# Optimization experiments

Measured on AMD Instinct MI355X. Metric: run time of the kernel, lower is better.

Reference implementation:

```python
import jax, jax.numpy as jnp
import numpy as np

B, N, HIST, PRED = 32, 4096, 16, 8
IN_DIM, HID, GCN_OUT, E = 10, 32, 2, 65536


def setup_inputs() -> dict:
    key = jax.random.key(0)
    ks = jax.random.split(key, 11)
    s = 0.15  # keep gate pre-activations in a sane range
    return {
        "pm25_hist": jax.random.normal(ks[0], (B, HIST, N), jnp.float32),
        "feature": jax.random.normal(ks[1], (B, HIST + PRED, N, IN_DIM - 1), jnp.float32),
        "edge_index": jax.random.randint(ks[2], (2, E), 0, N, dtype=jnp.int32),
        "cheb_w": jax.random.normal(ks[3], (2, IN_DIM, GCN_OUT), jnp.float32) * s,
        "cheb_b": jax.random.normal(ks[4], (GCN_OUT,), jnp.float32) * s,
        "x2h_w": jax.random.normal(ks[5], (IN_DIM + GCN_OUT, 4 * HID), jnp.float32) * s,
        "x2h_b": jax.random.normal(ks[6], (4 * HID,), jnp.float32) * s,
        "h2h_w": jax.random.normal(ks[7], (HID, 4 * HID), jnp.float32) * s,
        "h2h_b": jax.random.normal(ks[8], (4 * HID,), jnp.float32) * s,
        "fc_w": jax.random.normal(ks[9], (HID, 1), jnp.float32) * s,
        "fc_b": jax.random.normal(ks[10], (1,), jnp.float32) * s,
    }


def _cheb_norm(edge_index):
    # PyG ChebConv(K=2, sym norm, lambda_max=2): Tx1 = -D^{-1/2} A D^{-1/2} x, zero diagonal
    src, dst = edge_index[0], edge_index[1]
    deg = jnp.zeros((N,), jnp.float32).at[src].add(1.0)
    dis = jnp.where(deg > 0, jax.lax.rsqrt(jnp.maximum(deg, 1e-12)), 0.0)
    return -dis[src] * dis[dst], src, dst


def _cheb_conv(x, src, dst, norm, W, b):
    # x: [B,N,F]; message x[src] aggregated at dst
    msg = x[:, src, :] * norm[None, :, None]
    tx1 = jnp.zeros_like(x[..., :1].repeat(x.shape[-1], -1)).at[:, dst, :].add(msg)
    return jnp.einsum("bnf,fo->bno", x, W[0]) + jnp.einsum("bnf,fo->bno", tx1, W[1]) + b


def _lstm(x, h, c, x2h_w, x2h_b, h2h_w, h2h_b):
    g = x @ x2h_w + x2h_b + h @ h2h_w + h2h_b  # [B,N,4H]
    i, f, gc, o = jnp.split(g, 4, axis=-1)
    c = jax.nn.sigmoid(f) * c + jax.nn.sigmoid(i) * jnp.tanh(gc)
    h = jax.nn.sigmoid(o) * jnp.tanh(c)
    return h, c


def reference(pm25_hist, feature, edge_index, cheb_w, cheb_b, x2h_w, x2h_b, h2h_w, h2h_b, fc_w, fc_b):
    norm, src, dst = _cheb_norm(edge_index)

    def step(carry, x):
        h, c = carry
        xg = jax.nn.sigmoid(_cheb_conv(x, src, dst, norm, cheb_w, cheb_b))
        h, c = _lstm(jnp.concatenate([x, xg], -1), h, c, x2h_w, x2h_b, h2h_w, h2h_b)
        return (h, c), None

    h = jnp.zeros((B, N, HID), jnp.float32)
    c = jnp.zeros((B, N, HID), jnp.float32)

    # history phase
    xs_hist = jnp.concatenate([pm25_hist[..., None], feature[:, :HIST]], -1)  # [B,HIST,N,10]
    (h, c), _ = jax.lax.scan(step, (h, c), jnp.swapaxes(xs_hist, 0, 1))
    xn = h @ fc_w + fc_b  # [B,N,1]

    # prediction phase (recurrent through xn)
    def pred_step(carry, feat_t):
        h, c, xn = carry
        x = jnp.concatenate([xn, feat_t], -1)  # [B,N,10]
        (h, c), _ = step((h, c), x)
        xn = h @ fc_w + fc_b
        return (h, c, xn), xn

    _, ys = jax.lax.scan(pred_step, (h, c, xn), jnp.swapaxes(feature[:, HIST:], 0, 1))
    return jnp.squeeze(jnp.swapaxes(ys, 0, 1), -1)  # [B,PRED,N]
```

## Files before the change

kernel.cpp:

```cpp
#include <hip/hip_runtime.h>
#include <math.h>

#define Bb    32
#define Nn    4096
#define HISTC 16
#define PREDC 8
#define TTC   24
#define EC    65536
#define BN    (Bb*Nn)

typedef float f32x2 __attribute__((ext_vector_type(2)));
typedef float f32x4 __attribute__((ext_vector_type(4)));
typedef __fp16 f16x8 __attribute__((ext_vector_type(8)));
typedef __fp16 fp16v2 __attribute__((ext_vector_type(2)));

__device__ __forceinline__ float sigm_f(float x){
  return __builtin_amdgcn_rcpf(1.f + __expf(-x));
}
__device__ __forceinline__ float tanh_f(float x){
  return fmaf(-2.f, __builtin_amdgcn_rcpf(1.f + __expf(2.f*x)), 1.f);
}
__device__ __forceinline__ unsigned pk2(float a, float b){
  fp16v2 v = __builtin_amdgcn_cvt_pkrtz(a, b);
  return __builtin_bit_cast(unsigned, v);
}
__device__ __forceinline__ f32x4 mfma16(uint4 a, uint4 b, f32x4 c){
  return __builtin_amdgcn_mfma_f32_16x16x32_f16(
      __builtin_bit_cast(f16x8, a), __builtin_bit_cast(f16x8, b), c, 0, 0, 0);
}

__global__ void k_deg(const int* __restrict__ ei, int* deg, int* cnt){
  int e = blockIdx.x*blockDim.x + threadIdx.x;
  if (e < EC){ atomicAdd(&deg[ei[e]],1); atomicAdd(&cnt[ei[EC+e]],1); }
}
__global__ void k_dis(const int* __restrict__ deg, float* dis){
  int n = blockIdx.x*blockDim.x + threadIdx.x;
  if (n < Nn) dis[n] = deg[n] > 0 ? rsqrtf((float)deg[n]) : 0.f;
}
__global__ void k_scan(const int* __restrict__ cnt, int* ptr){
  __shared__ int sd[1024];
  int t = threadIdx.x;
  int c0=cnt[4*t], c1=cnt[4*t+1], c2=cnt[4*t+2], c3=cnt[4*t+3];
  int s = c0+c1+c2+c3;
  sd[t] = s; __syncthreads();
  for (int off=1; off<1024; off<<=1){
    int v = (t>=off) ? sd[t-off] : 0;
    __syncthreads();
    sd[t] += v;
    __syncthreads();
  }
  int excl = sd[t]-s;
  ptr[4*t]=excl; ptr[4*t+1]=excl+c0; ptr[4*t+2]=excl+c0+c1; ptr[4*t+3]=excl+c0+c1+c2;
  if (t==1023) ptr[4096]=sd[1023];
}
__global__ void k_fill(const int* __restrict__ ei, const float* __restrict__ dis,
                       const int* __restrict__ ptr, int* fillc, int2* __restrict__ epack){
  int e = blockIdx.x*blockDim.x + threadIdx.x;
  if (e < EC){
    int s = ei[e], d = ei[EC+e];
    int pos = ptr[d] + atomicAdd(&fillc[d],1);
    epack[pos] = make_int2(s, __float_as_int(-dis[s]*dis[d]));
  }
}

__global__ void k_prep(const float* __restrict__ x2hw, const float* __restrict__ h2hw,
                       const float* __restrict__ x2hb, const float* __restrict__ h2hb,
                       _Float16* __restrict__ wfrag){
  int i = blockIdx.x*256 + threadIdx.x;
  int f = i >> 9, lane = (i >> 3) & 63, j = i & 7;
  int kt = f >> 3, ct = f & 7;
  int k = kt*32 + (lane>>4)*8 + j;
  int col = ct*16 + (lane&15);
  float v;
  if (k < 12)       v = x2hw[k*128 + col];
  else if (k == 12) v = x2hb[col] + h2hb[col];
  else if (k < 32)  v = 0.f;
  else              v = h2hw[(k-32)*128 + col];
  wfrag[f*512 + lane*8 + j] = (_Float16)v;
}

__global__ __launch_bounds__(256)
void k_zh(const float* __restrict__ pm25, const float* __restrict__ feat,
          const float* __restrict__ cw, f32x2* __restrict__ zbufH){
  int r = blockIdx.x*256 + threadIdx.x;
  int t = r >> 17, bn = r & (BN-1);
  int b = bn >> 12, n = bn & (Nn-1);
  const float* fp = feat + ((size_t)(b*TTC + t)*Nn + n)*9;
  float x[10];
  x[0] = pm25[(size_t)(b*HISTC + t)*Nn + n];
  #pragma unroll
  for (int f=0;f<9;++f) x[1+f] = fp[f];
  float z0=0.f, z1=0.f;
  #pragma unroll
  for (int f=0;f<10;++f){
    z0 += x[f]*cw[20+f*2+0]; z1 += x[f]*cw[20+f*2+1];
  }
  zbufH[((size_t)(t*Bb + b))*Nn + n] = (f32x2){z0, z1};
}

__global__ __launch_bounds__(256)
void k_tr(const f32x2* __restrict__ in, f32x2* __restrict__ out, int R, int C){
  __shared__ f32x2 tile[64][65];
  int tilesR = R >> 6;
  int br = blockIdx.x % tilesR, bc = blockIdx.x / tilesR;
  int r0 = br << 6, c0 = bc << 6;
  for (int i=threadIdx.x; i<4096; i+=256){
    int r = i>>6, c = i&63;
    tile[r][c] = in[(size_t)(r0+r)*C + c0+c];
  }
  __syncthreads();
  for (int i=threadIdx.x; i<4096; i+=256){
    int r = i>>6, c = i&63;
    out[(size_t)(c0+r)*R + r0+c] = tile[c][r];
  }
}

__global__ __launch_bounds__(256)
void k_agg(const int* __restrict__ ptr, const int2* __restrict__ epack,
           const float4* __restrict__ zT, float4* __restrict__ aggT){
  int n = blockIdx.x;
  int tid = threadIdx.x;
  int p0 = ptr[n], p1 = ptr[n+1];
  f32x4 acc = {0.f,0.f,0.f,0.f};
  int i = p0;
  for (; i+1 < p1; i += 2){
    int2 e0 = epack[i], e1 = epack[i+1];
    float w0 = __int_as_float(e0.y), w1 = __int_as_float(e1.y);
    float4 z0 = zT[(size_t)e0.x*256 + tid];
    float4 z1 = zT[(size_t)e1.x*256 + tid];
    acc.x = fmaf(w0, z0.x, acc.x); acc.y = fmaf(w0, z0.y, acc.y);
    acc.z = fmaf(w0, z0.z, acc.z); acc.w = fmaf(w0, z0.w, acc.w);
    acc.x = fmaf(w1, z1.x, acc.x); acc.y = fmaf(w1, z1.y, acc.y);
    acc.z = fmaf(w1, z1.z, acc.z); acc.w = fmaf(w1, z1.w, acc.w);
  }
  if (i < p1){
    int2 e = epack[i];
    float w = __int_as_float(e.y);
    float4 z = zT[(size_t)e.x*256 + tid];
    acc.x = fmaf(w, z.x, acc.x); acc.y = fmaf(w, z.y, acc.y);
    acc.z = fmaf(w, z.z, acc.z); acc.w = fmaf(w, z.w, acc.w);
  }
  aggT[(size_t)n*256 + tid] = make_float4(acc.x, acc.y, acc.z, acc.w);
}

__global__ __launch_bounds__(256)
void k_zf(const float* __restrict__ feat, const float* __restrict__ cw,
          f32x2* __restrict__ zf){
  int r = blockIdx.x*256 + threadIdx.x;
  int tp = r >> 17, bn = r & (BN-1);
  int b = bn >> 12, n = bn & (Nn-1);
  int t = HISTC + tp;
  const float* fp = feat + ((size_t)(b*TTC + t)*Nn + n)*9;
  float z0=0.f, z1=0.f;
  #pragma unroll
  for (int f=0;f<9;++f){
    float v = fp[f];
    z0 += v*cw[20+(f+1)*2+0]; z1 += v*cw[20+(f+1)*2+1];
  }
  zf[((size_t)(tp*Bb + b))*Nn + n] = (f32x2){z0, z1};
}

#define POINTWISE(r)                                                            \
  c0[r] = fmaf(sigm_f(acc[0][r]), tanh_f(acc[4][r]), sigm_f(acc[2][r])*c0[r]);  \
  h0[r] = sigm_f(acc[6][r])*tanh_f(c0[r]);                                      \
  c1[r] = fmaf(sigm_f(acc[1][r]), tanh_f(acc[5][r]), sigm_f(acc[3][r])*c1[r]);  \
  h1[r] = sigm_f(acc[7][r])*tanh_f(c1[r]);

__global__ __launch_bounds__(256,1)
void k_hist(const float* __restrict__ pm25, const float* __restrict__ feat,
            const f32x2* __restrict__ aggH,
            const float* __restrict__ cw, const float* __restrict__ cb,
            const uint4* __restrict__ wfrag,
            const float* __restrict__ fcw, const float* __restrict__ fcb,
            uint4* __restrict__ hfragO, float4* __restrict__ cO,
            float* __restrict__ xn0){
  __shared__ __align__(16) _Float16 hl[4][16][40];
  int tid = threadIdx.x;
  int lane = tid & 63, w = tid >> 6;
  int gw = blockIdx.x*4 + w;
  int r0 = gw*16;
  int b = r0 >> 12, n0 = r0 & (Nn-1);
  int l15 = lane & 15, g4 = lane >> 4;
  int nrow = n0 + l15;
  const float* pb = pm25 + (size_t)b*HISTC*Nn + nrow;
  const float* fb = feat + ((size_t)b*TTC*Nn + nrow)*9;

  uint4 bw[16];
  #pragma unroll
  for (int f=0; f<16; ++f) bw[f] = wfrag[f*64 + lane];
  float fw0 = fcw[l15], fw1 = fcw[l15+16];

  uint4 ah = make_uint4(0,0,0,0);
  float c0[4]={0,0,0,0}, c1[4]={0,0,0,0};
  float h0[4], h1[4];
  const f32x4 zacc = {0.f,0.f,0.f,0.f};

  #pragma unroll 1
  for (int t=0; t<HISTC; ++t){
    const float* fbt = fb + (size_t)t*Nn*9;
    float xv[9]; float a0 = 0.f, a1 = 0.f; float x0 = 0.f;
    if (g4 == 0){
      x0 = pb[(size_t)t*Nn];
      #pragma unroll
      for (int f=0;f<7;++f) xv[f] = fbt[f];
      a0 = x0*cw[0]; a1 = x0*cw[1];
      #pragma unroll
      for (int f=0;f<7;++f){ a0 += xv[f]*cw[(f+1)*2]; a1 += xv[f]*cw[(f+1)*2+1]; }
    } else if (g4 == 1){
      xv[7] = fbt[7]; xv[8] = fbt[8];
      a0 = cb[0] + xv[7]*cw[16] + xv[8]*cw[18];
      a1 = cb[1] + xv[7]*cw[17] + xv[8]*cw[19];
    } else if (g4 == 2){
      f32x2 ag = aggH[((size_t)(t*Bb + b))*Nn + nrow];
      a0 = ag.x; a1 = ag.y;
    }
    a0 += __shfl_xor(a0, 16); a0 += __shfl_xor(a0, 32);
    a1 += __shfl_xor(a1, 16); a1 += __shfl_xor(a1, 32);
    float xg0 = sigm_f(a0), xg1 = sigm_f(a1);

    uint4 ax;
    if (g4 == 0){
      ax.x = pk2(x0, xv[0]);     ax.y = pk2(xv[1], xv[2]);
      ax.z = pk2(xv[3], xv[4]);  ax.w = pk2(xv[5], xv[6]);
    } else if (g4 == 1){
      ax.x = pk2(xv[7], xv[8]);  ax.y = pk2(xg0, xg1);
      ax.z = pk2(1.f, 0.f);      ax.w = 0u;
    } else {
      ax = make_uint4(0,0,0,0);
    }

    f32x4 acc[8];
    #pragma unroll
    for (int ct=0; ct<8; ++ct) acc[ct] = mfma16(ax, bw[ct], zacc);
    #pragma unroll
    for (int ct=0; ct<8; ++ct) acc[ct] = mfma16(ah, bw[8+ct], acc[ct]);

    POINTWISE(0) POINTWISE(1) POINTWISE(2) POINTWISE(3)

    #pragma unroll
    for (int r=0;r<4;++r){
      hl[w][g4*4+r][l15]    = (_Float16)h0[r];
      hl[w][g4*4+r][l15+16] = (_Float16)h1[r];
    }
    asm volatile("s_waitcnt lgkmcnt(0)" ::: "memory");
    ah = *(const uint4*)&hl[w][l15][g4*8];
  }

  hfragO[(size_t)gw*64 + lane] = ah;
  cO[((size_t)gw*64 + lane)*2]   = make_float4(c0[0],c0[1],c0[2],c0[3]);
  cO[((size_t)gw*64 + lane)*2+1] = make_float4(c1[0],c1[1],c1[2],c1[3]);
  #pragma unroll
  for (int r=0;r<4;++r){
    float p = fmaf(h0[r], fw0, h1[r]*fw1);
    p += __shfl_xor(p, 1, 16); p += __shfl_xor(p, 2, 16);
    p += __shfl_xor(p, 4, 16); p += __shfl_xor(p, 8, 16);
    if (l15 == 0) xn0[r0 + g4*4 + r] = p + fcb[0];
  }
}

__global__ __launch_bounds__(256,1)
void k_pred_cell(const float* __restrict__ feat, const float* __restrict__ xnI,
                 const f32x2* __restrict__ zft,
                 const int* __restrict__ ptr, const int2* __restrict__ epack,
                 const float* __restrict__ cw, const float* __restrict__ cb,
                 const uint4* __restrict__ wfrag,
                 const float* __restrict__ fcw, const float* __restrict__ fcb,
                 uint4* __restrict__ hfrag, float4* __restrict__ cS,
                 float* __restrict__ xnO, float* __restrict__ out, int t){
  __shared__ f32x2 zl2[Nn];
  __shared__ __align__(16) _Float16 hl[4][16][40];
  int tid = threadIdx.x;
  int lane = tid & 63, w = tid >> 6;
  int gw = blockIdx.x*4 + w;
  int r0 = gw*16;
  int b = r0 >> 12, n0 = r0 & (Nn-1);
  int l15 = lane & 15, g4 = lane >> 4;

  {
    const f32x2* zsrc = zft + (size_t)b*Nn;
    const float* xb = xnI + (size_t)b*Nn;
    float w10 = cw[20], w11 = cw[21];
    #pragma unroll
    for (int k=0;k<16;++k){
      int idx = tid + k*256;
      f32x2 z = zsrc[idx];
      float xnv = xb[idx];
      zl2[idx] = (f32x2){fmaf(xnv, w10, z.x), fmaf(xnv, w11, z.y)};
    }
  }

  uint4 bw[16];
  #pragma unroll
  for (int f=0; f<16; ++f) bw[f] = wfrag[f*64 + lane];
  float fw0 = fcw[l15], fw1 = fcw[l15+16];

  uint4 ah = hfrag[(size_t)gw*64 + lane];
  float4 cv0 = cS[((size_t)gw*64 + lane)*2];
  float4 cv1 = cS[((size_t)gw*64 + lane)*2+1];
  float c0[4] = {cv0.x, cv0.y, cv0.z, cv0.w};
  float c1[4] = {cv1.x, cv1.y, cv1.z, cv1.w};
  float h0[4], h1[4];
  const f32x4 zacc = {0.f,0.f,0.f,0.f};

  int nrow = n0 + l15;
  const float* fbt = feat + ((size_t)(b*TTC + t)*Nn + n0 + l15)*9;
  float xv[9]; float a0 = 0.f, a1 = 0.f; float x0 = 0.f;
  if (g4 == 0){
    x0 = xnI[r0 + l15];
    #pragma unroll
    for (int f=0;f<7;++f) xv[f] = fbt[f];
    a0 = x0*cw[0]; a1 = x0*cw[1];
    #pragma unroll
    for (int f=0;f<7;++f){ a0 += xv[f]*cw[(f+1)*2]; a1 += xv[f]*cw[(f+1)*2+1]; }
  } else if (g4 == 1){
    xv[7] = fbt[7]; xv[8] = fbt[8];
    a0 = cb[0] + xv[7]*cw[16] + xv[8]*cw[18];
    a1 = cb[1] + xv[7]*cw[17] + xv[8]*cw[19];
  }

  __syncthreads();

  {
    int p0 = ptr[nrow], p1 = ptr[nrow+1];
    for (int i = p0 + g4; i < p1; i += 4){
      int2 e = epack[i];
      float wgt = __int_as_float(e.y);
      f32x2 zv = zl2[e.x];
      a0 = fmaf(wgt, zv.x, a0);
      a1 = fmaf(wgt, zv.y, a1);
    }
    a0 += __shfl_xor(a0, 16); a0 += __shfl_xor(a0, 32);
    a1 += __shfl_xor(a1, 16); a1 += __shfl_xor(a1, 32);
  }
  float xg0 = sigm_f(a0), xg1 = sigm_f(a1);

  uint4 ax;
  if (g4 == 0){
    ax.x = pk2(x0, xv[0]);     ax.y = pk2(xv[1], xv[2]);
    ax.z = pk2(xv[3], xv[4]);  ax.w = pk2(xv[5], xv[6]);
  } else if (g4 == 1){
    ax.x = pk2(xv[7], xv[8]);  ax.y = pk2(xg0, xg1);
    ax.z = pk2(1.f, 0.f);      ax.w = 0u;
  } else {
    ax = make_uint4(0,0,0,0);
  }

  f32x4 acc[8];
  #pragma unroll
  for (int ct=0; ct<8; ++ct) acc[ct] = mfma16(ax, bw[ct], zacc);
  #pragma unroll
  for (int ct=0; ct<8; ++ct) acc[ct] = mfma16(ah, bw[8+ct], acc[ct]);

  POINTWISE(0) POINTWISE(1) POINTWISE(2) POINTWISE(3)

  #pragma unroll
  for (int r=0;r<4;++r){
    hl[w][g4*4+r][l15]    = (_Float16)h0[r];
    hl[w][g4*4+r][l15+16] = (_Float16)h1[r];
  }
  asm volatile("s_waitcnt lgkmcnt(0)" ::: "memory");
  ah = *(const uint4*)&hl[w][l15][g4*8];

  hfrag[(size_t)gw*64 + lane] = ah;
  cS[((size_t)gw*64 + lane)*2]   = make_float4(c0[0],c0[1],c0[2],c0[3]);
  cS[((size_t)gw*64 + lane)*2+1] = make_float4(c1[0],c1[1],c1[2],c1[3]);
  #pragma unroll
  for (int r=0;r<4;++r){
    float p = fmaf(h0[r], fw0, h1[r]*fw1);
    p += __shfl_xor(p, 1, 16); p += __shfl_xor(p, 2, 16);
    p += __shfl_xor(p, 4, 16); p += __shfl_xor(p, 8, 16);
    if (l15 == 0){
      float rr = p + fcb[0];
      int nr = n0 + g4*4 + r;
      xnO[r0 + g4*4 + r] = rr;
      out[(size_t)b*PREDC*Nn + nr] = rr;
    }
  }
}

extern "C" void kernel_launch(void* const* d_in, const int* in_sizes, int n_in,
                              void* d_out, int out_size, void* d_ws, size_t ws_size,
                              hipStream_t stream){
  const float* pm25 = (const float*)d_in[0];
  const float* feat = (const float*)d_in[1];
  const int*   ei   = (const int*)d_in[2];
  const float* cw   = (const float*)d_in[3];
  const float* cb   = (const float*)d_in[4];
  const float* x2hw = (const float*)d_in[5];
  const float* x2hb = (const float*)d_in[6];
  const float* h2hw = (const float*)d_in[7];
  const float* h2hb = (const float*)d_in[8];
  const float* fcw  = (const float*)d_in[9];
  const float* fcb  = (const float*)d_in[10];
  float* out = (float*)d_out;

  char* w = (char*)d_ws;
  size_t off = 0;
  auto take = [&](size_t bytes)->char*{
    char* r = w + off; off += (bytes + 255) & ~(size_t)255; return r;
  };
  int*      deg   = (int*)      take(Nn*4);
  int*      cnt   = (int*)      take(Nn*4);
  int*      fillc = (int*)      take(Nn*4);
  int*      ptr   = (int*)      take((Nn+1)*4);
  float*    dis   = (float*)    take(Nn*4);
  int2*     epack = (int2*)     take(EC*8);
  _Float16* wfrag = (_Float16*) take(16*512*2);
  f32x2*    bufA  = (f32x2*)    take((size_t)HISTC*BN*8);
  f32x2*    bufB  = (f32x2*)    take((size_t)HISTC*BN*8);
  f32x2*    zf    = (f32x2*)    take((size_t)PREDC*BN*8);
  uint4*    hfrag = (uint4*)    take((size_t)(BN/16)*64*16);
  float4*   cbuf  = (float4*)   take((size_t)(BN/16)*64*2*16);
  float*    xn0   = (float*)    take((size_t)BN*4);
  float*    xn1   = (float*)    take((size_t)BN*4);

  (void)hipMemsetAsync(deg, 0, Nn*4*3, stream);

  k_deg <<<EC/256, 256, 0, stream>>>(ei, deg, cnt);
  k_dis <<<Nn/256, 256, 0, stream>>>(deg, dis);
  k_scan<<<1, 1024, 0, stream>>>(cnt, ptr);
  k_fill<<<EC/256, 256, 0, stream>>>(ei, dis, ptr, fillc, epack);
  k_prep<<<32, 256, 0, stream>>>(x2hw, h2hw, x2hb, h2hb, wfrag);

  k_zh<<<(HISTC*BN)/256, 256, 0, stream>>>(pm25, feat, cw, bufA);
  k_tr<<<512, 256, 0, stream>>>(bufA, bufB, 512, Nn);
  k_agg<<<Nn, 256, 0, stream>>>(ptr, epack, (const float4*)bufB, (float4*)bufA);
  k_tr<<<512, 256, 0, stream>>>(bufA, bufB, Nn, 512);

  k_hist<<<BN/64, 256, 0, stream>>>(pm25, feat, bufB, cw, cb,
                                    (const uint4*)wfrag, fcw, fcb,
                                    hfrag, cbuf, xn0);

  k_zf<<<(PREDC*BN)/256, 256, 0, stream>>>(feat, cw, zf);
  for (int tp = 0; tp < PREDC; ++tp){
    int t = HISTC + tp;
    float* xi = (tp & 1) ? xn1 : xn0;
    float* xo = (tp & 1) ? xn0 : xn1;
    k_pred_cell<<<BN/64, 256, 0, stream>>>(feat, xi, zf + (size_t)tp*BN,
                                           ptr, epack, cw, cb,
                                           (const uint4*)wfrag, fcw, fcb,
                                           hfrag, cbuf, xo, out + (size_t)tp*Nn, t);
  }
}
```

Before: 436.2 us.

## Precompute feature-part graph aggregation for prediction steps and aggregate only xn per step

Uses linearity of the Chebyshev aggregation to split each prediction step's graph term into a feature part and an xn part. The feature part is computed for all 8 prediction steps in one batched transpose/aggregate pass alongside the history steps, and each step then only aggregates the scalar xn via a small k_aggx kernel using a transposed xn layout. This replaces the per-block shared-memory z staging and edge loop in k_pred_cell. k_hist now processes two row tiles per wave, and buffers are aliased to cut workspace size, at the cost of an extra kernel launch per prediction step.

```diff
diff --git a/kernel.cpp b/kernel.cpp
--- a/kernel.cpp
+++ b/kernel.cpp
@@ -8,6 +8,7 @@
 #define TTC   24
 #define EC    65536
 #define BN    (Bb*Nn)
+#define NSL   768
 
 typedef float f32x2 __attribute__((ext_vector_type(2)));
 typedef float f32x4 __attribute__((ext_vector_type(4)));
@@ -81,7 +82,7 @@
 
 __global__ __launch_bounds__(256)
 void k_zh(const float* __restrict__ pm25, const float* __restrict__ feat,
-          const float* __restrict__ cw, f32x2* __restrict__ zbufH){
+          const float* __restrict__ cw, f32x2* __restrict__ zAll){
   int r = blockIdx.x*256 + threadIdx.x;
   int t = r >> 17, bn = r & (BN-1);
   int b = bn >> 12, n = bn & (Nn-1);
@@ -95,7 +96,24 @@
   for (int f=0;f<10;++f){
     z0 += x[f]*cw[20+f*2+0]; z1 += x[f]*cw[20+f*2+1];
   }
-  zbufH[((size_t)(t*Bb + b))*Nn + n] = (f32x2){z0, z1};
+  zAll[((size_t)(t*Bb + b))*Nn + n] = (f32x2){z0, z1};
+}
+
+__global__ __launch_bounds__(256)
+void k_zf(const float* __restrict__ feat, const float* __restrict__ cw,
+          f32x2* __restrict__ zAll){
+  int r = blockIdx.x*256 + threadIdx.x;
+  int tp = r >> 17, bn = r & (BN-1);
+  int b = bn >> 12, n = bn & (Nn-1);
+  int t = HISTC + tp;
+  const float* fp = feat + ((size_t)(b*TTC + t)*Nn + n)*9;
+  float z0=0.f, z1=0.f;
+  #pragma unroll
+  for (int f=0;f<9;++f){
+    float v = fp[f];
+    z0 += v*cw[20+(f+1)*2+0]; z1 += v*cw[20+(f+1)*2+1];
+  }
+  zAll[((size_t)(512 + tp*Bb + b))*Nn + n] = (f32x2){z0, z1};
 }
 
 __global__ __launch_bounds__(256)
@@ -115,19 +133,20 @@
   }
 }
 
-__global__ __launch_bounds__(256)
-void k_agg(const int* __restrict__ ptr, const int2* __restrict__ epack,
-           const float4* __restrict__ zT, float4* __restrict__ aggT){
-  int n = blockIdx.x;
-  int tid = threadIdx.x;
+__global__ __launch_bounds__(64)
+void k_aggc(const int* __restrict__ ptr, const int2* __restrict__ epack,
+            const float4* __restrict__ zT, float4* __restrict__ aggT){
+  int n  = blockIdx.x & (Nn-1);
+  int cb = blockIdx.x >> 12;
+  int col = cb*64 + threadIdx.x;
   int p0 = ptr[n], p1 = ptr[n+1];
   f32x4 acc = {0.f,0.f,0.f,0.f};
   int i = p0;
   for (; i+1 < p1; i += 2){
     int2 e0 = epack[i], e1 = epack[i+1];
     float w0 = __int_as_float(e0.y), w1 = __int_as_float(e1.y);
-    float4 z0 = zT[(size_t)e0.x*256 + tid];
-    float4 z1 = zT[(size_t)e1.x*256 + tid];
+    float4 z0 = zT[(size_t)e0.x*384 + col];
+    float4 z1 = zT[(size_t)e1.x*384 + col];
     acc.x = fmaf(w0, z0.x, acc.x); acc.y = fmaf(w0, z0.y, acc.y);
     acc.z = fmaf(w0, z0.z, acc.z); acc.w = fmaf(w0, z0.w, acc.w);
     acc.x = fmaf(w1, z1.x, acc.x); acc.y = fmaf(w1, z1.y, acc.y);
@@ -136,28 +155,27 @@
   if (i < p1){
     int2 e = epack[i];
     float w = __int_as_float(e.y);
-    float4 z = zT[(size_t)e.x*256 + tid];
+    float4 z = zT[(size_t)e.x*384 + col];
     acc.x = fmaf(w, z.x, acc.x); acc.y = fmaf(w, z.y, acc.y);
     acc.z = fmaf(w, z.z, acc.z); acc.w = fmaf(w, z.w, acc.w);
   }
-  aggT[(size_t)n*256 + tid] = make_float4(acc.x, acc.y, acc.z, acc.w);
+  aggT[(size_t)n*384 + col] = make_float4(acc.x, acc.y, acc.z, acc.w);
 }
 
 __global__ __launch_bounds__(256)
-void k_zf(const float* __restrict__ feat, const float* __restrict__ cw,
-          f32x2* __restrict__ zf){
-  int r = blockIdx.x*256 + threadIdx.x;
-  int tp = r >> 17, bn = r & (BN-1);
-  int b = bn >> 12, n = bn & (Nn-1);
-  int t = HISTC + tp;
-  const float* fp = feat + ((size_t)(b*TTC + t)*Nn + n)*9;
-  float z0=0.f, z1=0.f;
-  #pragma unroll
-  for (int f=0;f<9;++f){
-    float v = fp[f];
-    z0 += v*cw[20+(f+1)*2+0]; z1 += v*cw[20+(f+1)*2+1];
-  }
-  zf[((size_t)(tp*Bb + b))*Nn + n] = (f32x2){z0, z1};
+void k_aggx(const int* __restrict__ ptr, const int2* __restrict__ epack,
+            const float* __restrict__ xnT, float* __restrict__ aggx){
+  int lane = threadIdx.x & 63, w = threadIdx.x >> 6;
+  int n = blockIdx.x*4 + w;
+  int b = lane & 31, half = lane >> 5;
+  int p0 = ptr[n], p1 = ptr[n+1];
+  float acc = 0.f;
+  for (int i = p0 + half; i < p1; i += 2){
+    int2 e = epack[i];
+    acc = fmaf(__int_as_float(e.y), xnT[(size_t)e.x*32 + b], acc);
+  }
+  acc += __shfl_xor(acc, 32);
+  if (lane < 32) aggx[(size_t)b*Nn + n] = acc;
 }
 
 #define POINTWISE(r)                                                            \
@@ -173,7 +191,110 @@
             const uint4* __restrict__ wfrag,
             const float* __restrict__ fcw, const float* __restrict__ fcb,
             uint4* __restrict__ hfragO, float4* __restrict__ cO,
-            float* __restrict__ xn0){
+            float* __restrict__ xn0, float* __restrict__ xnT){
+  __shared__ __align__(16) _Float16 hl[4][16][40];
+  int tid = threadIdx.x;
+  int lane = tid & 63, w = tid >> 6;
+  int gw0 = blockIdx.x*4 + w;
+  int l15 = lane & 15, g4 = lane >> 4;
+
+  uint4 bw[16];
+  #pragma unroll
+  for (int f=0; f<16; ++f) bw[f] = wfrag[f*64 + lane];
+  float fw0 = fcw[l15], fw1 = fcw[l15+16];
+  const f32x4 zacc = {0.f,0.f,0.f,0.f};
+
+  #pragma unroll 1
+  for (int tt=0; tt<2; ++tt){
+    int gw = gw0 + tt*4096;
+    int r0 = gw*16;
+    int b = r0 >> 12, n0 = r0 & (Nn-1);
+    int nrow = n0 + l15;
+    const float* pb = pm25 + (size_t)b*HISTC*Nn + nrow;
+    const float* fb = feat + ((size_t)b*TTC*Nn + nrow)*9;
+
+    uint4 ah = make_uint4(0,0,0,0);
+    float c0[4]={0,0,0,0}, c1[4]={0,0,0,0};
+    float h0[4], h1[4];
+
+    #pragma unroll 1
+    for (int t=0; t<HISTC; ++t){
+      const float* fbt = fb + (size_t)t*Nn*9;
+      float xv[9]; float a0 = 0.f, a1 = 0.f; float x0 = 0.f;
+      if (g4 == 0){
+        x0 = pb[(size_t)t*Nn];
+        #pragma unroll
+        for (int f=0;f<7;++f) xv[f] = fbt[f];
+        a0 = x0*cw[0]; a1 = x0*cw[1];
+        #pragma unroll
+        for (int f=0;f<7;++f){ a0 += xv[f]*cw[(f+1)*2]; a1 += xv[f]*cw[(f+1)*2+1]; }
+      } else if (g4 == 1){
+        xv[7] = fbt[7]; xv[8] = fbt[8];
+        a0 = cb[0] + xv[7]*cw[16] + xv[8]*cw[18];
+        a1 = cb[1] + xv[7]*cw[17] + xv[8]*cw[19];
+      } else if (g4 == 2){
+        f32x2 ag = aggH[((size_t)(t*Bb + b))*Nn + nrow];
+        a0 = ag.x; a1 = ag.y;
+      }
+      a0 += __shfl_xor(a0, 16); a0 += __shfl_xor(a0, 32);
+      a1 += __shfl_xor(a1, 16); a1 += __shfl_xor(a1, 32);
+      float xg0 = sigm_f(a0), xg1 = sigm_f(a1);
+
+      uint4 ax;
+      if (g4 == 0){
+        ax.x = pk2(x0, xv[0]);     ax.y = pk2(xv[1], xv[2]);
+        ax.z = pk2(xv[3], xv[4]);  ax.w = pk2(xv[5], xv[6]);
+      } else if (g4 == 1){
+        ax.x = pk2(xv[7], xv[8]);  ax.y = pk2(xg0, xg1);
+        ax.z = pk2(1.f, 0.f);      ax.w = 0u;
+      } else {
+        ax = make_uint4(0,0,0,0);
+      }
+
+      f32x4 acc[8];
+      #pragma unroll
+      for (int ct=0; ct<8; ++ct) acc[ct] = mfma16(ax, bw[ct], zacc);
+      #pragma unroll
+      for (int ct=0; ct<8; ++ct) acc[ct] = mfma16(ah, bw[8+ct], acc[ct]);
+
+      POINTWISE(0) POINTWISE(1) POINTWISE(2) POINTWISE(3)
+
+      #pragma unroll
+      for (int r=0;r<4;++r){
+        hl[w][g4*4+r][l15]    = (_Float16)h0[r];
+        hl[w][g4*4+r][l15+16] = (_Float16)h1[r];
+      }
+      asm volatile("s_waitcnt lgkmcnt(0)" ::: "memory");
+      ah = *(const uint4*)&hl[w][l15][g4*8];
+    }
+
+    hfragO[(size_t)gw*64 + lane] = ah;
+    cO[((size_t)gw*64 + lane)*2]   = make_float4(c0[0],c0[1],c0[2],c0[3]);
+    cO[((size_t)gw*64 + lane)*2+1] = make_float4(c1[0],c1[1],c1[2],c1[3]);
+    #pragma unroll
+    for (int r=0;r<4;++r){
+      float p = fmaf(h0[r], fw0, h1[r]*fw1);
+      p += __shfl_xor(p, 1, 16); p += __shfl_xor(p, 2, 16);
+      p += __shfl_xor(p, 4, 16); p += __shfl_xor(p, 8, 16);
+      if (l15 == 0){
+        float rr = p + fcb[0];
+        int nr = n0 + g4*4 + r;
+        xn0[r0 + g4*4 + r] = rr;
+        xnT[(size_t)nr*32 + b] = rr;
+      }
+    }
+  }
+}
+
+__global__ __launch_bounds__(256,1)
+void k_pred_cell(const float* __restrict__ feat, float* __restrict__ xn0,
+                 const f32x2* __restrict__ aggzf,
+                 const float* __restrict__ aggx,
+                 const float* __restrict__ cw, const float* __restrict__ cb,
+                 const uint4* __restrict__ wfrag,
+                 const float* __restrict__ fcw, const float* __restrict__ fcb,
+                 uint4* __restrict__ hfrag, float4* __restrict__ cS,
+                 float* __restrict__ xnT, float* __restrict__ out, int t){
   __shared__ __align__(16) _Float16 hl[4][16][40];
   int tid = threadIdx.x;
   int lane = tid & 63, w = tid >> 6;
@@ -182,112 +303,6 @@
   int b = r0 >> 12, n0 = r0 & (Nn-1);
   int l15 = lane & 15, g4 = lane >> 4;
   int nrow = n0 + l15;
-  const float* pb = pm25 + (size_t)b*HISTC*Nn + nrow;
-  const float* fb = feat + ((size_t)b*TTC*Nn + nrow)*9;
-
-  uint4 bw[16];
-  #pragma unroll
-  for (int f=0; f<16; ++f) bw[f] = wfrag[f*64 + lane];
-  float fw0 = fcw[l15], fw1 = fcw[l15+16];
-
-  uint4 ah = make_uint4(0,0,0,0);
-  float c0[4]={0,0,0,0}, c1[4]={0,0,0,0};
-  float h0[4], h1[4];
-  const f32x4 zacc = {0.f,0.f,0.f,0.f};
-
-  #pragma unroll 1
-  for (int t=0; t<HISTC; ++t){
-    const float* fbt = fb + (size_t)t*Nn*9;
-    float xv[9]; float a0 = 0.f, a1 = 0.f; float x0 = 0.f;
-    if (g4 == 0){
-      x0 = pb[(size_t)t*Nn];
-      #pragma unroll
-      for (int f=0;f<7;++f) xv[f] = fbt[f];
-      a0 = x0*cw[0]; a1 = x0*cw[1];
-      #pragma unroll
-      for (int f=0;f<7;++f){ a0 += xv[f]*cw[(f+1)*2]; a1 += xv[f]*cw[(f+1)*2+1]; }
-    } else if (g4 == 1){
-      xv[7] = fbt[7]; xv[8] = fbt[8];
-      a0 = cb[0] + xv[7]*cw[16] + xv[8]*cw[18];
-      a1 = cb[1] + xv[7]*cw[17] + xv[8]*cw[19];
-    } else if (g4 == 2){
-      f32x2 ag = aggH[((size_t)(t*Bb + b))*Nn + nrow];
-      a0 = ag.x; a1 = ag.y;
-    }
-    a0 += __shfl_xor(a0, 16); a0 += __shfl_xor(a0, 32);
-    a1 += __shfl_xor(a1, 16); a1 += __shfl_xor(a1, 32);
-    float xg0 = sigm_f(a0), xg1 = sigm_f(a1);
-
-    uint4 ax;
-    if (g4 == 0){
-      ax.x = pk2(x0, xv[0]);     ax.y = pk2(xv[1], xv[2]);
-      ax.z = pk2(xv[3], xv[4]);  ax.w = pk2(xv[5], xv[6]);
-    } else if (g4 == 1){
-      ax.x = pk2(xv[7], xv[8]);  ax.y = pk2(xg0, xg1);
-      ax.z = pk2(1.f, 0.f);      ax.w = 0u;
-    } else {
-      ax = make_uint4(0,0,0,0);
-    }
-
-    f32x4 acc[8];
-    #pragma unroll
-    for (int ct=0; ct<8; ++ct) acc[ct] = mfma16(ax, bw[ct], zacc);
-    #pragma unroll
-    for (int ct=0; ct<8; ++ct) acc[ct] = mfma16(ah, bw[8+ct], acc[ct]);
-
-    POINTWISE(0) POINTWISE(1) POINTWISE(2) POINTWISE(3)
-
-    #pragma unroll
-    for (int r=0;r<4;++r){
-      hl[w][g4*4+r][l15]    = (_Float16)h0[r];
-      hl[w][g4*4+r][l15+16] = (_Float16)h1[r];
-    }
-    asm volatile("s_waitcnt lgkmcnt(0)" ::: "memory");
-    ah = *(const uint4*)&hl[w][l15][g4*8];
-  }
-
-  hfragO[(size_t)gw*64 + lane] = ah;
-  cO[((size_t)gw*64 + lane)*2]   = make_float4(c0[0],c0[1],c0[2],c0[3]);
-  cO[((size_t)gw*64 + lane)*2+1] = make_float4(c1[0],c1[1],c1[2],c1[3]);
-  #pragma unroll
-  for (int r=0;r<4;++r){
-    float p = fmaf(h0[r], fw0, h1[r]*fw1);
-    p += __shfl_xor(p, 1, 16); p += __shfl_xor(p, 2, 16);
-    p += __shfl_xor(p, 4, 16); p += __shfl_xor(p, 8, 16);
-    if (l15 == 0) xn0[r0 + g4*4 + r] = p + fcb[0];
-  }
-}
-
-__global__ __launch_bounds__(256,1)
-void k_pred_cell(const float* __restrict__ feat, const float* __restrict__ xnI,
-                 const f32x2* __restrict__ zft,
-                 const int* __restrict__ ptr, const int2* __restrict__ epack,
-                 const float* __restrict__ cw, const float* __restrict__ cb,
-                 const uint4* __restrict__ wfrag,
-                 const float* __restrict__ fcw, const float* __restrict__ fcb,
-                 uint4* __restrict__ hfrag, float4* __restrict__ cS,
-                 float* __restrict__ xnO, float* __restrict__ out, int t){
-  __shared__ f32x2 zl2[Nn];
-  __shared__ __align__(16) _Float16 hl[4][16][40];
-  int tid = threadIdx.x;
-  int lane = tid & 63, w = tid >> 6;
-  int gw = blockIdx.x*4 + w;
-  int r0 = gw*16;
-  int b = r0 >> 12, n0 = r0 & (Nn-1);
-  int l15 = lane & 15, g4 = lane >> 4;
-
-  {
-    const f32x2* zsrc = zft + (size_t)b*Nn;
-    const float* xb = xnI + (size_t)b*Nn;
-    float w10 = cw[20], w11 = cw[21];
-    #pragma unroll
-    for (int k=0;k<16;++k){
-      int idx = tid + k*256;
-      f32x2 z = zsrc[idx];
-      float xnv = xb[idx];
-      zl2[idx] = (f32x2){fmaf(xnv, w10, z.x), fmaf(xnv, w11, z.y)};
-    }
-  }
 
   uint4 bw[16];
   #pragma unroll
@@ -302,11 +317,10 @@
   float h0[4], h1[4];
   const f32x4 zacc = {0.f,0.f,0.f,0.f};
 
-  int nrow = n0 + l15;
-  const float* fbt = feat + ((size_t)(b*TTC + t)*Nn + n0 + l15)*9;
+  const float* fbt = feat + ((size_t)(b*TTC + t)*Nn + nrow)*9;
   float xv[9]; float a0 = 0.f, a1 = 0.f; float x0 = 0.f;
   if (g4 == 0){
-    x0 = xnI[r0 + l15];
+    x0 = xn0[r0 + l15];
     #pragma unroll
     for (int f=0;f<7;++f) xv[f] = fbt[f];
     a0 = x0*cw[0]; a1 = x0*cw[1];
@@ -316,22 +330,14 @@
     xv[7] = fbt[7]; xv[8] = fbt[8];
     a0 = cb[0] + xv[7]*cw[16] + xv[8]*cw[18];
     a1 = cb[1] + xv[7]*cw[17] + xv[8]*cw[19];
-  }
-
-  __syncthreads();
-
-  {
-    int p0 = ptr[nrow], p1 = ptr[nrow+1];
-    for (int i = p0 + g4; i < p1; i += 4){
-      int2 e = epack[i];
-      float wgt = __int_as_float(e.y);
-      f32x2 zv = zl2[e.x];
-      a0 = fmaf(wgt, zv.x, a0);
-      a1 = fmaf(wgt, zv.y, a1);
-    }
-    a0 += __shfl_xor(a0, 16); a0 += __shfl_xor(a0, 32);
-    a1 += __shfl_xor(a1, 16); a1 += __shfl_xor(a1, 32);
-  }
+  } else if (g4 == 2){
+    f32x2 azf = aggzf[(size_t)b*Nn + nrow];
+    float axv = aggx[(size_t)b*Nn + nrow];
+    a0 = fmaf(cw[20], axv, azf.x);
+    a1 = fmaf(cw[21], axv, azf.y);
+  }
+  a0 += __shfl_xor(a0, 16); a0 += __shfl_xor(a0, 32);
+  a1 += __shfl_xor(a1, 16); a1 += __shfl_xor(a1, 32);
   float xg0 = sigm_f(a0), xg1 = sigm_f(a1);
 
   uint4 ax;
@@ -372,7 +378,8 @@
     if (l15 == 0){
       float rr = p + fcb[0];
       int nr = n0 + g4*4 + r;
-      xnO[r0 + g4*4 + r] = rr;
+      xn0[r0 + g4*4 + r] = rr;
+      xnT[(size_t)nr*32 + b] = rr;
       out[(size_t)b*PREDC*Nn + nr] = rr;
     }
   }
@@ -394,10 +401,10 @@
   const float* fcb  = (const float*)d_in[10];
   float* out = (float*)d_out;
 
-  char* w = (char*)d_ws;
+  char* wsp = (char*)d_ws;
   size_t off = 0;
   auto take = [&](size_t bytes)->char*{
-    char* r = w + off; off += (bytes + 255) & ~(size_t)255; return r;
+    char* r = wsp + off; off += (bytes + 255) & ~(size_t)255; return r;
   };
   int*      deg   = (int*)      take(Nn*4);
   int*      cnt   = (int*)      take(Nn*4);
@@ -406,13 +413,16 @@
   float*    dis   = (float*)    take(Nn*4);
   int2*     epack = (int2*)     take(EC*8);
   _Float16* wfrag = (_Float16*) take(16*512*2);
-  f32x2*    bufA  = (f32x2*)    take((size_t)HISTC*BN*8);
-  f32x2*    bufB  = (f32x2*)    take((size_t)HISTC*BN*8);
-  f32x2*    zf    = (f32x2*)    take((size_t)PREDC*BN*8);
-  uint4*    hfrag = (uint4*)    take((size_t)(BN/16)*64*16);
-  float4*   cbuf  = (float4*)   take((size_t)(BN/16)*64*2*16);
+  char*     bufA  =             take((size_t)NSL*Nn*8);
+  char*     bufB  =             take((size_t)NSL*Nn*8);
   float*    xn0   = (float*)    take((size_t)BN*4);
-  float*    xn1   = (float*)    take((size_t)BN*4);
+  float*    xnT   = (float*)    take((size_t)BN*4);
+  float*    aggx  = (float*)    take((size_t)BN*4);
+
+  f32x2* zAll = (f32x2*)bufA;
+  f32x2* zT   = (f32x2*)bufB;
+  uint4*  hfrag = (uint4*)bufA;
+  float4* cbuf  = (float4*)(bufA + (size_t)8388608);
 
   (void)hipMemsetAsync(deg, 0, Nn*4*3, stream);
 
@@ -422,23 +432,24 @@
   k_fill<<<EC/256, 256, 0, stream>>>(ei, dis, ptr, fillc, epack);
   k_prep<<<32, 256, 0, stream>>>(x2hw, h2hw, x2hb, h2hb, wfrag);
 
-  k_zh<<<(HISTC*BN)/256, 256, 0, stream>>>(pm25, feat, cw, bufA);
-  k_tr<<<512, 256, 0, stream>>>(bufA, bufB, 512, Nn);
-  k_agg<<<Nn, 256, 0, stream>>>(ptr, epack, (const float4*)bufB, (float4*)bufA);
-  k_tr<<<512, 256, 0, stream>>>(bufA, bufB, Nn, 512);
-
-  k_hist<<<BN/64, 256, 0, stream>>>(pm25, feat, bufB, cw, cb,
-                                    (const uint4*)wfrag, fcw, fcb,
-                                    hfrag, cbuf, xn0);
-
-  k_zf<<<(PREDC*BN)/256, 256, 0, stream>>>(feat, cw, zf);
+  k_zh<<<(HISTC*BN)/256, 256, 0, stream>>>(pm25, feat, cw, zAll);
+  k_zf<<<(PREDC*BN)/256, 256, 0, stream>>>(feat, cw, zAll);
+  k_tr<<<(NSL/64)*(Nn/64), 256, 0, stream>>>(zAll, zT, NSL, Nn);
+  k_aggc<<<6*Nn, 64, 0, stream>>>(ptr, epack, (const float4*)zT, (float4*)zAll);
+  k_tr<<<(Nn/64)*(NSL/64), 256, 0, stream>>>((const f32x2*)zAll, (f32x2*)bufB, Nn, NSL);
+
+  const f32x2* aggAll = (const f32x2*)bufB;
+
+  k_hist<<<BN/128, 256, 0, stream>>>(pm25, feat, aggAll, cw, cb,
+                                     (const uint4*)wfrag, fcw, fcb,
+                                     hfrag, cbuf, xn0, xnT);
+
   for (int tp = 0; tp < PREDC; ++tp){
     int t = HISTC + tp;
-    float* xi = (tp & 1) ? xn1 : xn0;
-    float* xo = (tp & 1) ? xn0 : xn1;
-    k_pred_cell<<<BN/64, 256, 0, stream>>>(feat, xi, zf + (size_t)tp*BN,
-                                           ptr, epack, cw, cb,
-                                           (const uint4*)wfrag, fcw, fcb,
-                                           hfrag, cbuf, xo, out + (size_t)tp*Nn, t);
-  }
-}
+    k_aggx<<<Nn/4, 256, 0, stream>>>(ptr, epack, xnT, aggx);
+    k_pred_cell<<<BN/64, 256, 0, stream>>>(feat, xn0,
+                                           aggAll + (size_t)(512 + tp*Bb)*Nn, aggx,
+                                           cw, cb, (const uint4*)wfrag, fcw, fcb,
+                                           hfrag, cbuf, xnT, out + (size_t)tp*Nn, t);
+  }
+}
```

Result: slower. 461.7 us (+5.8%).
